# Kernel optimization log

Measured on AMD Instinct MI355X. Metric: run time of the kernel, lower is better.

Reference implementation:

```python
import jax, jax.numpy as jnp
import numpy as np

N_NODES = 8192
N_EDGES = 262144
IN_DIM = 256
HID = 256
OUT_DIM = 64
PATH_DIM = 64
N_HEADS = 4


def setup_inputs() -> dict:
    key = jax.random.key(0)
    ks = jax.random.split(key, 16)
    s = 0.05
    x = jax.random.normal(ks[0], (N_NODES, IN_DIM), dtype=jnp.float32)
    edge_index = jax.random.randint(ks[1], (2, N_EDGES), 0, N_NODES, dtype=jnp.int32)
    return {
        "x": x,
        "edge_index": edge_index,
        # pathway encoder Linear(IN_DIM, PATH_DIM)
        "pe_w": jax.random.normal(ks[2], (IN_DIM, PATH_DIM), jnp.float32) * s,
        "pe_b": jax.random.normal(ks[3], (PATH_DIM,), jnp.float32) * s,
        # MultiheadAttention packed in-proj [3E, E] and out-proj [E, E]
        "in_proj_w": jax.random.normal(ks[4], (3 * PATH_DIM, PATH_DIM), jnp.float32) * s,
        "in_proj_b": jax.random.normal(ks[5], (3 * PATH_DIM,), jnp.float32) * s,
        "out_proj_w": jax.random.normal(ks[6], (PATH_DIM, PATH_DIM), jnp.float32) * s,
        "out_proj_b": jax.random.normal(ks[7], (PATH_DIM,), jnp.float32) * s,
        # GCN layer weights (in_dim, out_dim) + bias
        "w1": jax.random.normal(ks[8], (IN_DIM + PATH_DIM, HID), jnp.float32) * s,
        "b1": jax.random.normal(ks[9], (HID,), jnp.float32) * s,
        "w2": jax.random.normal(ks[10], (HID, HID), jnp.float32) * s,
        "b2": jax.random.normal(ks[11], (HID,), jnp.float32) * s,
        "w3": jax.random.normal(ks[12], (HID, OUT_DIM), jnp.float32) * s,
        "b3": jax.random.normal(ks[13], (OUT_DIM,), jnp.float32) * s,
    }


def mha_self(x, in_proj_w, in_proj_b, out_proj_w, out_proj_b):
    # unbatched nn.MultiheadAttention: x [N, E], Q=K=V=x
    N, E = x.shape
    dh = E // N_HEADS
    qkv = x @ in_proj_w.T + in_proj_b  # [N, 3E]
    q, k, v = jnp.split(qkv, 3, axis=-1)
    # [H, N, dh]
    q = q.reshape(N, N_HEADS, dh).transpose(1, 0, 2)
    k = k.reshape(N, N_HEADS, dh).transpose(1, 0, 2)
    v = v.reshape(N, N_HEADS, dh).transpose(1, 0, 2)
    scores = jnp.einsum('hnd,hmd->hnm', q, k) / jnp.sqrt(jnp.float32(dh))
    attn = jax.nn.softmax(scores, axis=-1)
    out = jnp.einsum('hnm,hmd->hnd', attn, v)  # [H, N, dh]
    out = out.transpose(1, 0, 2).reshape(N, E)
    return out @ out_proj_w.T + out_proj_b


def gcn_conv(h, edge_index, w, b, num_nodes):
    # PyG GCNConv: add self loops, symmetric normalization, linear, scatter-add, bias
    src = jnp.concatenate([edge_index[0], jnp.arange(num_nodes, dtype=edge_index.dtype)])
    dst = jnp.concatenate([edge_index[1], jnp.arange(num_nodes, dtype=edge_index.dtype)])
    deg = jax.ops.segment_sum(jnp.ones_like(dst, dtype=h.dtype), dst, num_segments=num_nodes)
    dinv = jnp.where(deg > 0, jax.lax.rsqrt(jnp.maximum(deg, 1e-12)), 0.0)
    hw = h @ w  # [N, out]
    norm = (dinv[src] * dinv[dst])[:, None]
    msg = hw[src] * norm
    out = jax.ops.segment_sum(msg, dst, num_segments=num_nodes)
    return out + b


def reference(x, edge_index, pe_w, pe_b, in_proj_w, in_proj_b, out_proj_w, out_proj_b,
              w1, b1, w2, b2, w3, b3):
    N = x.shape[0]
    pf = x @ pe_w + pe_b  # pathway encoder
    pa = mha_self(pf, in_proj_w, in_proj_b, out_proj_w, out_proj_b)
    h = jnp.concatenate([x, pa], axis=-1)  # [N, IN_DIM + PATH_DIM]
    h = jax.nn.relu(gcn_conv(h, edge_index, w1, b1, N))  # dropout is identity (eval)
    h = jax.nn.relu(gcn_conv(h, edge_index, w2, b2, N))
    h = gcn_conv(h, edge_index, w3, b3, N)
    return h
```

## Files before the change

kernel.cpp:

```cpp
#include <hip/hip_runtime.h>
#include <hip/hip_bf16.h>

#define N_NODES 8192
#define N_EDGES 262144
#define IN_DIM 256
#define HID 256
#define OUT_DIM 64
#define PATH_DIM 64
#define NHEADS 4
#define DH 16
#define KSPLIT 8
#define SPLIT_KEYS (N_NODES / KSPLIT)
#define NITER (SPLIT_KEYS / 64)

typedef __attribute__((ext_vector_type(8))) short bf16x8;
typedef __attribute__((ext_vector_type(4))) short bf16x4;
typedef __attribute__((ext_vector_type(4))) float f32x4;

__device__ __forceinline__ ushort f2bf(float f) {
  union { float f; unsigned int u; } c;
  c.f = f;
  unsigned int u = c.u;
  u += 0x7fffu + ((u >> 16) & 1u);
  return (ushort)(u >> 16);
}

__device__ __forceinline__ float bf2f(ushort u) {
  union { float f; unsigned int u; } c;
  c.u = ((unsigned int)u) << 16;
  return c.f;
}

__device__ __forceinline__ float fast_exp2(float x) {
  float r;
  asm("v_exp_f32 %0, %1" : "=v"(r) : "v"(x));
  return r;
}

__device__ __forceinline__ unsigned pack_bf16(float a, float b) {
  union { __hip_bfloat162 h; unsigned u; } c;
  c.h = __float22bfloat162_rn(make_float2(a, b));
  return c.u;
}

#if __has_builtin(__builtin_amdgcn_mfma_f32_16x16x16bf16_1k)
__device__ __forceinline__ f32x4 mfma16(bf16x4 a, bf16x4 b, f32x4 c) {
  return __builtin_amdgcn_mfma_f32_16x16x16bf16_1k(a, b, c, 0, 0, 0);
}
#else
__device__ __forceinline__ f32x4 mfma16(bf16x4 a, bf16x4 b, f32x4 c) {
  f32x4 d;
  asm volatile("v_mfma_f32_16x16x16_bf16 %0, %1, %2, %3\n\ts_nop 7\n\ts_nop 3"
               : "=v"(d) : "v"(a), "v"(b), "v"(c));
  return d;
}
#endif


__global__ __launch_bounds__(256) void init_graph(int* deg, int* cursor) {
  int i = blockIdx.x * 256 + threadIdx.x;
  if (i < N_NODES) { deg[i] = 1; cursor[i] = 0; }
}

__global__ __launch_bounds__(256) void count_deg(const int* __restrict__ dst,
                                                 int* __restrict__ deg) {
  int e = blockIdx.x * 256 + threadIdx.x;
  if (e < N_EDGES) atomicAdd(&deg[dst[e]], 1);
}

__global__ __launch_bounds__(256) void scan_rows(const int* __restrict__ deg,
                                                 int* __restrict__ row_off,
                                                 float* __restrict__ dinv) {
  __shared__ int part[256];
  int t = threadIdx.x;
  int base = t * 32;
  int local[32];
  int s = 0;
  #pragma unroll
  for (int i = 0; i < 32; ++i) {
    int c = deg[base + i] - 1;
    local[i] = s;
    s += c;
  }
  part[t] = s;
  __syncthreads();
  for (int d = 1; d < 256; d <<= 1) {
    int v = (t >= d) ? part[t - d] : 0;
    __syncthreads();
    part[t] += v;
    __syncthreads();
  }
  int prev = (t == 0) ? 0 : part[t - 1];
  #pragma unroll
  for (int i = 0; i < 32; ++i) {
    row_off[base + i] = prev + local[i];
    dinv[base + i] = rsqrtf((float)deg[base + i]);
  }
}

__global__ __launch_bounds__(256) void fill_csr(const int* __restrict__ src,
                                                const int* __restrict__ dst,
                                                const int* __restrict__ row_off,
                                                int* __restrict__ cursor,
                                                int* __restrict__ csr) {
  int e = blockIdx.x * 256 + threadIdx.x;
  if (e < N_EDGES) {
    int d = dst[e];
    int p = atomicAdd(&cursor[d], 1);
    csr[row_off[d] + p] = src[e];
  }
}


__global__ __launch_bounds__(256) void transpose_w(const float* __restrict__ W,
                                                   float* __restrict__ Wt,
                                                   int R, int C) {
  int i = blockIdx.x * 256 + threadIdx.x;
  if (i < R * C) {
    int r = i / C, c = i % C;
    Wt[c * R + r] = W[i];
  }
}

__global__ __launch_bounds__(256) void convert_wsplit(const float* __restrict__ W,
                                                      ushort* __restrict__ Bthi,
                                                      ushort* __restrict__ Btlo,
                                                      int K, int N) {
  int i = blockIdx.x * 256 + threadIdx.x;
  if (i < K * N) {
    int k = i / N, n = i % N;
    float v = W[i];
    ushort hi = f2bf(v);
    ushort lo = f2bf(v - bf2f(hi));
    Bthi[(size_t)n * K + k] = hi;
    Btlo[(size_t)n * K + k] = lo;
  }
}

__global__ __launch_bounds__(256) void convert_xpa(const float* __restrict__ x,
                                                   const float* __restrict__ pa,
                                                   ushort* __restrict__ Axpa) {
  int i = blockIdx.x * 256 + threadIdx.x;
  int n = i / 80;
  int c = (i % 80) * 4;
  float4 v;
  if (c < 256)
    v = *reinterpret_cast<const float4*>(x + (size_t)n * 256 + c);
  else
    v = *reinterpret_cast<const float4*>(pa + (size_t)n * 64 + (c - 256));
  *reinterpret_cast<ushort4*>(Axpa + (size_t)n * 320 + c) =
      make_ushort4(f2bf(v.x), f2bf(v.y), f2bf(v.z), f2bf(v.w));
}

__global__ __launch_bounds__(256) void convert_qkv(const float* __restrict__ qkv,
                                                   ushort* __restrict__ Qbf,
                                                   ushort* __restrict__ Kbf,
                                                   ushort* __restrict__ Vtb) {
  const int tg = blockIdx.x * 256 + threadIdx.x;
  const int h = tg >> 13;
  const int n = tg & 8191;
  const float SC = 0.36067376022224085f;
  const float* base = qkv + (size_t)n * 192 + h * 16;
  ushort* qd = Qbf + ((size_t)h * 8192 + n) * 32;
  ushort* kd = Kbf + ((size_t)h * 8192 + n) * 32;
  ushort4 zz = make_ushort4(0, 0, 0, 0);
  #pragma unroll
  for (int i = 0; i < 16; i += 4) {
    float4 q4 = *reinterpret_cast<const float4*>(base + i);
    float4 k4 = *reinterpret_cast<const float4*>(base + 64 + i);
    float4 v4 = *reinterpret_cast<const float4*>(base + 128 + i);
    *reinterpret_cast<ushort4*>(qd + i) =
        make_ushort4(f2bf(q4.x * SC), f2bf(q4.y * SC), f2bf(q4.z * SC), f2bf(q4.w * SC));
    *reinterpret_cast<ushort4*>(kd + i) =
        make_ushort4(f2bf(k4.x), f2bf(k4.y), f2bf(k4.z), f2bf(k4.w));
    *reinterpret_cast<ushort4*>(qd + 16 + i) = zz;
    *reinterpret_cast<ushort4*>(kd + 16 + i) = zz;
    Vtb[((size_t)h * 16 + i + 0) * 8192 + n] = f2bf(v4.x);
    Vtb[((size_t)h * 16 + i + 1) * 8192 + n] = f2bf(v4.y);
    Vtb[((size_t)h * 16 + i + 2) * 8192 + n] = f2bf(v4.z);
    Vtb[((size_t)h * 16 + i + 3) * 8192 + n] = f2bf(v4.w);
  }
}


template <bool RELU, bool BIAS>
__global__ __launch_bounds__(256) void gemm_tile(const float* __restrict__ A1, int K1,
                                                 const float* __restrict__ A2, int K2,
                                                 const float* __restrict__ B,
                                                 const float* __restrict__ bias,
                                                 float* __restrict__ C, int N) {
  __shared__ __align__(16) float As[16][64];
  __shared__ __align__(16) float Bs[16][68];
  const int K = K1 + K2;
  const int bm = blockIdx.y * 64;
  const int bn = blockIdx.x * 64;
  const int t = threadIdx.x;
  const int tx = t & 15, ty = t >> 4;
  const int am = t >> 2;
  const int ak = (t & 3) << 2;
  const int bk = t >> 4;
  const int bn4 = (t & 15) << 2;
  float acc[4][4] = {};
  for (int k0 = 0; k0 < K; k0 += 16) {
    int kk = k0 + ak;
    int row = bm + am;
    float4 av;
    if (kk < K1)
      av = *reinterpret_cast<const float4*>(A1 + (size_t)row * K1 + kk);
    else
      av = *reinterpret_cast<const float4*>(A2 + (size_t)row * K2 + (kk - K1));
    As[ak + 0][am] = av.x;
    As[ak + 1][am] = av.y;
    As[ak + 2][am] = av.z;
    As[ak + 3][am] = av.w;
    float4 bv = *reinterpret_cast<const float4*>(B + (size_t)(k0 + bk) * N + bn + bn4);
    *reinterpret_cast<float4*>(&Bs[bk][bn4]) = bv;
    __syncthreads();
    #pragma unroll
    for (int k = 0; k < 16; ++k) {
      float4 a = *reinterpret_cast<const float4*>(&As[k][ty << 2]);
      float4 b = *reinterpret_cast<const float4*>(&Bs[k][tx << 2]);
      acc[0][0] += a.x * b.x; acc[0][1] += a.x * b.y; acc[0][2] += a.x * b.z; acc[0][3] += a.x * b.w;
      acc[1][0] += a.y * b.x; acc[1][1] += a.y * b.y; acc[1][2] += a.y * b.z; acc[1][3] += a.y * b.w;
      acc[2][0] += a.z * b.x; acc[2][1] += a.z * b.y; acc[2][2] += a.z * b.z; acc[2][3] += a.z * b.w;
      acc[3][0] += a.w * b.x; acc[3][1] += a.w * b.y; acc[3][2] += a.w * b.z; acc[3][3] += a.w * b.w;
    }
    __syncthreads();
  }
  #pragma unroll
  for (int i = 0; i < 4; ++i) {
    int row = bm + (ty << 2) + i;
    float4 o = make_float4(acc[i][0], acc[i][1], acc[i][2], acc[i][3]);
    if (BIAS) {
      float4 bv = *reinterpret_cast<const float4*>(bias + bn + (tx << 2));
      o.x += bv.x; o.y += bv.y; o.z += bv.z; o.w += bv.w;
    }
    if (RELU) {
      o.x = fmaxf(o.x, 0.f); o.y = fmaxf(o.y, 0.f);
      o.z = fmaxf(o.z, 0.f); o.w = fmaxf(o.w, 0.f);
    }
    *reinterpret_cast<float4*>(C + (size_t)row * N + bn + (tx << 2)) = o;
  }
}


template <int K, int NT>
__global__ __launch_bounds__(256) void gemm_mfma(const ushort* __restrict__ A,
                                                 const ushort* __restrict__ Bthi,
                                                 const ushort* __restrict__ Btlo,
                                                 ushort* __restrict__ C) {
  const int t = threadIdx.x;
  const int wv = t >> 6;
  const int l = t & 63;
  const int lg = l >> 4;
  const int lc = l & 15;
  const int bm = blockIdx.y * 64;
  const int n = blockIdx.x * 64 + wv * 16 + lc;

  const ushort* ap = A + (size_t)(bm + lc) * K + lg * 8;
  const ushort* bh = Bthi + (size_t)n * K + lg * 8;
  const ushort* bl = Btlo + (size_t)n * K + lg * 8;

  f32x4 acc[4] = {{0.f,0.f,0.f,0.f},{0.f,0.f,0.f,0.f},{0.f,0.f,0.f,0.f},{0.f,0.f,0.f,0.f}};
  #pragma unroll 2
  for (int k0 = 0; k0 < K; k0 += 32) {
    bf16x8 vh = *reinterpret_cast<const bf16x8*>(bh + k0);
    bf16x8 vl = *reinterpret_cast<const bf16x8*>(bl + k0);
    #pragma unroll
    for (int mt = 0; mt < 4; ++mt) {
      bf16x8 af = *reinterpret_cast<const bf16x8*>(ap + (size_t)mt * 16 * K + k0);
      acc[mt] = __builtin_amdgcn_mfma_f32_16x16x32_bf16(af, vh, acc[mt], 0, 0, 0);
      acc[mt] = __builtin_amdgcn_mfma_f32_16x16x32_bf16(af, vl, acc[mt], 0, 0, 0);
    }
  }
  #pragma unroll
  for (int mt = 0; mt < 4; ++mt) {
    #pragma unroll
    for (int r = 0; r < 4; ++r)
      C[(size_t)(bm + mt * 16 + lg * 4 + r) * NT + n] = f2bf(acc[mt][r]);
  }
}


__global__ __launch_bounds__(256) void attn_mfma5(const ushort* __restrict__ Qbf,
                                                  const ushort* __restrict__ Kbf,
                                                  const ushort* __restrict__ Vtb,
                                                  float* __restrict__ Opart,
                                                  float* __restrict__ Wpart) {
  const int h  = blockIdx.y;
  const int qb = blockIdx.x;
  const int kz = blockIdx.z;
  const int t  = threadIdx.x;
  const int wv = t >> 6;
  const int l  = t & 63;
  const int lg = l >> 4;
  const int lc = l & 15;

  __shared__ float red_o[3][64][17];
  __shared__ float red_w[3][64];

  bf16x8 qf[4];
  {
    const ushort* qbase = Qbf + ((size_t)h * 8192 + qb * 64) * 32;
    #pragma unroll
    for (int qt = 0; qt < 4; ++qt)
      qf[qt] = *reinterpret_cast<const bf16x8*>(qbase + (qt * 16 + lc) * 32 + lg * 8);
  }

  const ushort* kptr =
      Kbf + ((size_t)h * 8192 + kz * SPLIT_KEYS + wv * 16 + lc) * 32 + lg * 8;
  const ushort* vptr =
      Vtb + ((size_t)h * 16 + lc) * 8192 + kz * SPLIT_KEYS + wv * 16 + lg * 4;

  f32x4 oacc[4] = {{0.f, 0.f, 0.f, 0.f}, {0.f, 0.f, 0.f, 0.f},
                   {0.f, 0.f, 0.f, 0.f}, {0.f, 0.f, 0.f, 0.f}};
  float wsum[4] = {0.f, 0.f, 0.f, 0.f};

  bf16x8 kf = *reinterpret_cast<const bf16x8*>(kptr);
  bf16x4 vf = *reinterpret_cast<const bf16x4*>(vptr);

  for (int c = 0; c < NITER; ++c) {
    bf16x8 kf_n;
    bf16x4 vf_n;
    if (c + 1 < NITER) {
      kf_n = *reinterpret_cast<const bf16x8*>(kptr + (size_t)(c + 1) * 64 * 32);
      vf_n = *reinterpret_cast<const bf16x4*>(vptr + (size_t)(c + 1) * 64);
    }

    f32x4 s[4];
    #pragma unroll
    for (int qt = 0; qt < 4; ++qt) {
      f32x4 z = {0.f, 0.f, 0.f, 0.f};
      s[qt] = __builtin_amdgcn_mfma_f32_16x16x32_bf16(kf, qf[qt], z, 0, 0, 0);
    }

    #pragma unroll
    for (int qt = 0; qt < 4; ++qt) {
      float e0 = fast_exp2(s[qt][0]);
      float e1 = fast_exp2(s[qt][1]);
      float e2 = fast_exp2(s[qt][2]);
      float e3 = fast_exp2(s[qt][3]);
      wsum[qt] += (e0 + e1) + (e2 + e3);
      union { uint2 u; bf16x4 v; } pu;
      pu.u.x = pack_bf16(e0, e1);
      pu.u.y = pack_bf16(e2, e3);
      oacc[qt] = mfma16(pu.v, vf, oacc[qt]);
    }

    kf = kf_n;
    vf = vf_n;
  }

  #pragma unroll
  for (int qt = 0; qt < 4; ++qt) {
    float v = wsum[qt];
    v += __shfl_xor(v, 16);
    v += __shfl_xor(v, 32);
    wsum[qt] = v;
  }

  if (wv > 0) {
    #pragma unroll
    for (int qt = 0; qt < 4; ++qt) {
      #pragma unroll
      for (int r = 0; r < 4; ++r)
        red_o[wv - 1][qt * 16 + lg * 4 + r][lc] = oacc[qt][r];
      if (lg == 0) red_w[wv - 1][qt * 16 + lc] = wsum[qt];
    }
  }
  __syncthreads();

  if (wv == 0) {
    const size_t obase = ((size_t)(kz * NHEADS + h) * N_NODES + qb * 64);
    #pragma unroll
    for (int qt = 0; qt < 4; ++qt) {
      #pragma unroll
      for (int r = 0; r < 4; ++r) {
        const int q = qt * 16 + lg * 4 + r;
        float o = oacc[qt][r] + red_o[0][q][lc] + red_o[1][q][lc] + red_o[2][q][lc];
        Opart[(obase + q) * 16 + lc] = o;
      }
      if (lg == 0) {
        const int q = qt * 16 + lc;
        Wpart[obase + q] = wsum[qt] + red_w[0][q] + red_w[1][q] + red_w[2][q];
      }
    }
  }
}

__global__ __launch_bounds__(256) void attn_combine(const float* __restrict__ Opart,
                                                    const float* __restrict__ Wpart,
                                                    float* __restrict__ attn_out) {
  int i = blockIdx.x * 256 + threadIdx.x;
  int dq = i & 3;
  int hn = i >> 2;
  int h = hn >> 13;
  int n = hn & 8191;
  float4 acc = make_float4(0.f, 0.f, 0.f, 0.f);
  float ws = 0.f;
  #pragma unroll
  for (int s = 0; s < KSPLIT; ++s) {
    const size_t row = ((size_t)(s * NHEADS + h) * N_NODES + n);
    float4 v = *reinterpret_cast<const float4*>(Opart + row * 16 + dq * 4);
    acc.x += v.x; acc.y += v.y; acc.z += v.z; acc.w += v.w;
    ws += Wpart[row];
  }
  float inv = 1.f / ws;
  float4 o = make_float4(acc.x * inv, acc.y * inv, acc.z * inv, acc.w * inv);
  *reinterpret_cast<float4*>(attn_out + (size_t)n * 64 + h * 16 + dq * 4) = o;
}


template <bool RELU, bool OUTBF>
__global__ __launch_bounds__(256) void aggregate_bf(const ushort* __restrict__ hwb,
                                                    const int* __restrict__ csr,
                                                    const int* __restrict__ row_off,
                                                    const int* __restrict__ deg,
                                                    const float* __restrict__ dinv,
                                                    const float* __restrict__ bias,
                                                    ushort* __restrict__ outb,
                                                    float* __restrict__ outf) {
  __shared__ __align__(16) float part[2][256];
  const int t = threadIdx.x;
  const int rw = t >> 7;
  const int wh = (t >> 6) & 1;
  const int l = t & 63;
  const int r = blockIdx.x * 2 + rw;
  const float dr = dinv[r];
  const int off = row_off[r];
  const int cnt = deg[r] - 1;
  const int c = l << 2;

  float a0, a1, a2, a3;
  if (wh == 0) {
    ushort4 u = *reinterpret_cast<const ushort4*>(hwb + (size_t)r * 256 + c);
    a0 = dr * bf2f(u.x); a1 = dr * bf2f(u.y); a2 = dr * bf2f(u.z); a3 = dr * bf2f(u.w);
  } else {
    a0 = a1 = a2 = a3 = 0.f;
  }
  for (int e = wh; e < cnt; e += 2) {
    int s = csr[off + e];
    float wsc = dinv[s];
    ushort4 u = *reinterpret_cast<const ushort4*>(hwb + (size_t)s * 256 + c);
    a0 += wsc * bf2f(u.x); a1 += wsc * bf2f(u.y);
    a2 += wsc * bf2f(u.z); a3 += wsc * bf2f(u.w);
  }
  if (wh == 1)
    *reinterpret_cast<float4*>(&part[rw][c]) = make_float4(a0, a1, a2, a3);
  __syncthreads();
  if (wh == 0) {
    float4 p = *reinterpret_cast<const float4*>(&part[rw][c]);
    float4 bv = *reinterpret_cast<const float4*>(bias + c);
    float o0 = dr * (a0 + p.x) + bv.x;
    float o1 = dr * (a1 + p.y) + bv.y;
    float o2 = dr * (a2 + p.z) + bv.z;
    float o3 = dr * (a3 + p.w) + bv.w;
    if (RELU) {
      o0 = fmaxf(o0, 0.f); o1 = fmaxf(o1, 0.f);
      o2 = fmaxf(o2, 0.f); o3 = fmaxf(o3, 0.f);
    }
    if (OUTBF) {
      *reinterpret_cast<ushort4*>(outb + (size_t)r * 256 + c) =
          make_ushort4(f2bf(o0), f2bf(o1), f2bf(o2), f2bf(o3));
    } else {
      *reinterpret_cast<float4*>(outf + (size_t)r * 256 + c) =
          make_float4(o0, o1, o2, o3);
    }
  }
}

__global__ __launch_bounds__(256) void aggregate64_bf(const ushort* __restrict__ hwb,
                                                      const int* __restrict__ csr,
                                                      const int* __restrict__ row_off,
                                                      const int* __restrict__ deg,
                                                      const float* __restrict__ dinv,
                                                      const float* __restrict__ bias,
                                                      float* __restrict__ out) {
  const int w = threadIdx.x >> 6, l = threadIdx.x & 63;
  const int r = blockIdx.x * 4 + w;
  const float dr = dinv[r];
  const int off = row_off[r];
  const int cnt = deg[r] - 1;
  float a = dr * bf2f(hwb[(size_t)r * 64 + l]);
  for (int e = 0; e < cnt; ++e) {
    int s = csr[off + e];
    a += dinv[s] * bf2f(hwb[(size_t)s * 64 + l]);
  }
  out[(size_t)r * 64 + l] = dr * a + bias[l];
}


extern "C" void kernel_launch(void* const* d_in, const int* in_sizes, int n_in,
                              void* d_out, int out_size, void* d_ws, size_t ws_size,
                              hipStream_t stream) {
  const float* x          = (const float*)d_in[0];
  const int*   ei         = (const int*)d_in[1];
  const float* pe_w       = (const float*)d_in[2];
  const float* pe_b       = (const float*)d_in[3];
  const float* in_proj_w  = (const float*)d_in[4];
  const float* in_proj_b  = (const float*)d_in[5];
  const float* out_proj_w = (const float*)d_in[6];
  const float* out_proj_b = (const float*)d_in[7];
  const float* w1         = (const float*)d_in[8];
  const float* b1         = (const float*)d_in[9];
  const float* w2         = (const float*)d_in[10];
  const float* b2         = (const float*)d_in[11];
  const float* w3         = (const float*)d_in[12];
  const float* b3         = (const float*)d_in[13];

  const int* esrc = ei;
  const int* edst = ei + N_EDGES;

  char* ws = (char*)d_ws;
  size_t o = 0;
  auto take = [&](size_t n) {
    char* p = ws + o;
    o += (n + 255) & ~(size_t)255;
    return p;
  };
  float* pf       = (float*)take((size_t)N_NODES * PATH_DIM * 4);
  float* qkv      = (float*)take((size_t)N_NODES * 3 * PATH_DIM * 4);
  float* attn_out = (float*)take((size_t)N_NODES * PATH_DIM * 4);
  float* pa       = (float*)take((size_t)N_NODES * PATH_DIM * 4);
  char*  region1  = take(18874368);
  ushort* Qbf     = (ushort*)take((size_t)NHEADS * N_NODES * 32 * 2);
  ushort* Kbf     = (ushort*)take((size_t)NHEADS * N_NODES * 32 * 2);
  ushort* Vtb     = (ushort*)take((size_t)NHEADS * DH * N_NODES * 2);
  ushort* Bt1hi   = (ushort*)take((size_t)HID * 320 * 2);
  ushort* Bt1lo   = (ushort*)take((size_t)HID * 320 * 2);
  ushort* Bt2hi   = (ushort*)take((size_t)HID * HID * 2);
  ushort* Bt2lo   = (ushort*)take((size_t)HID * HID * 2);
  ushort* Bt3hi   = (ushort*)take((size_t)OUT_DIM * HID * 2);
  ushort* Bt3lo   = (ushort*)take((size_t)OUT_DIM * HID * 2);
  float* Wt_in    = (float*)take((size_t)3 * PATH_DIM * PATH_DIM * 4);
  float* Wt_out   = (float*)take((size_t)PATH_DIM * PATH_DIM * 4);
  float* dinv     = (float*)take((size_t)N_NODES * 4);
  int*   deg      = (int*)take((size_t)N_NODES * 4);
  int*   cursor   = (int*)take((size_t)N_NODES * 4);
  int*   row_off  = (int*)take((size_t)N_NODES * 4);
  int*   csr      = (int*)take((size_t)N_EDGES * 4);

  float* Opart = (float*)region1;
  float* Wpart = (float*)(region1 + 16777216);
  ushort* Axpa  = (ushort*)region1;
  ushort* hwbf  = Axpa + (size_t)N_NODES * 320;
  ushort* h1bf  = hwbf + (size_t)N_NODES * 256;
  ushort* h2bf  = h1bf + (size_t)N_NODES * 256;
  ushort* hw64  = h2bf + (size_t)N_NODES * 256;

  init_graph<<<N_NODES / 256, 256, 0, stream>>>(deg, cursor);
  count_deg<<<N_EDGES / 256, 256, 0, stream>>>(edst, deg);
  scan_rows<<<1, 256, 0, stream>>>(deg, row_off, dinv);
  fill_csr<<<N_EDGES / 256, 256, 0, stream>>>(esrc, edst, row_off, cursor, csr);

  transpose_w<<<(192 * 64 + 255) / 256, 256, 0, stream>>>(in_proj_w, Wt_in, 192, 64);
  transpose_w<<<(64 * 64 + 255) / 256, 256, 0, stream>>>(out_proj_w, Wt_out, 64, 64);
  convert_wsplit<<<(320 * 256 + 255) / 256, 256, 0, stream>>>(w1, Bt1hi, Bt1lo, 320, HID);
  convert_wsplit<<<(256 * 256 + 255) / 256, 256, 0, stream>>>(w2, Bt2hi, Bt2lo, HID, HID);
  convert_wsplit<<<(256 * 64 + 255) / 256, 256, 0, stream>>>(w3, Bt3hi, Bt3lo, HID, OUT_DIM);

  gemm_tile<false, true><<<dim3(1, 128), 256, 0, stream>>>(x, IN_DIM, nullptr, 0, pe_w, pe_b, pf, PATH_DIM);
  gemm_tile<false, true><<<dim3(3, 128), 256, 0, stream>>>(pf, PATH_DIM, nullptr, 0, Wt_in, in_proj_b, qkv, 3 * PATH_DIM);
  convert_qkv<<<(N_NODES * NHEADS) / 256, 256, 0, stream>>>(qkv, Qbf, Kbf, Vtb);
  attn_mfma5<<<dim3(128, 4, KSPLIT), 256, 0, stream>>>(Qbf, Kbf, Vtb, Opart, Wpart);
  attn_combine<<<(NHEADS * N_NODES * 4) / 256, 256, 0, stream>>>(Opart, Wpart, attn_out);
  gemm_tile<false, true><<<dim3(1, 128), 256, 0, stream>>>(attn_out, PATH_DIM, nullptr, 0, Wt_out, out_proj_b, pa, PATH_DIM);

  convert_xpa<<<(N_NODES * 80) / 256, 256, 0, stream>>>(x, pa, Axpa);
  gemm_mfma<320, 256><<<dim3(4, 128), 256, 0, stream>>>(Axpa, Bt1hi, Bt1lo, hwbf);
  aggregate_bf<true, true><<<N_NODES / 2, 256, 0, stream>>>(hwbf, csr, row_off, deg, dinv, b1, h1bf, nullptr);
  gemm_mfma<256, 256><<<dim3(4, 128), 256, 0, stream>>>(h1bf, Bt2hi, Bt2lo, hwbf);
  aggregate_bf<true, true><<<N_NODES / 2, 256, 0, stream>>>(hwbf, csr, row_off, deg, dinv, b2, h2bf, nullptr);
  gemm_mfma<256, 64><<<dim3(1, 128), 256, 0, stream>>>(h2bf, Bt3hi, Bt3lo, hw64);
  aggregate64_bf<<<N_NODES / 4, 256, 0, stream>>>(hw64, csr, row_off, deg, dinv, b3, (float*)d_out);
}
```

Before: 275.1 us.

## Fold pathway encoder into QKV projection and fuse prep and combine kernels

Pre-multiplies pe_w by in_proj_w, scaling the Q columns, so one GEMM from x produces Q/K/V directly in bf16 attention layouts. This drops the pf GEMM and the convert_qkv pass. The attention split-K combine is fused into the out-projection GEMM, which writes bf16 straight into the Axpa columns. Weight transposes and conversions plus the x-to-bf16 conversion are merged into a single prep launch. This cuts launches and intermediate fp32 round trips, but the QKV GEMM now has K=256 instead of 64 and the algebraic reassociation slightly changes rounding.

```diff
diff --git a/kernel.cpp b/kernel.cpp
--- a/kernel.cpp
+++ b/kernel.cpp
@@ -112,108 +112,96 @@
 }
 
 
-__global__ __launch_bounds__(256) void transpose_w(const float* __restrict__ W,
-                                                   float* __restrict__ Wt,
-                                                   int R, int C) {
-  int i = blockIdx.x * 256 + threadIdx.x;
-  if (i < R * C) {
-    int r = i / C, c = i % C;
-    Wt[c * R + r] = W[i];
-  }
-}
-
-__global__ __launch_bounds__(256) void convert_wsplit(const float* __restrict__ W,
-                                                      ushort* __restrict__ Bthi,
-                                                      ushort* __restrict__ Btlo,
-                                                      int K, int N) {
-  int i = blockIdx.x * 256 + threadIdx.x;
-  if (i < K * N) {
-    int k = i / N, n = i % N;
-    float v = W[i];
+__global__ __launch_bounds__(256) void prep(const float* __restrict__ x,
+                                            const float* __restrict__ pe_w,
+                                            const float* __restrict__ pe_b,
+                                            const float* __restrict__ in_proj_w,
+                                            const float* __restrict__ in_proj_b,
+                                            const float* __restrict__ out_proj_w,
+                                            const float* __restrict__ w1,
+                                            const float* __restrict__ w2,
+                                            const float* __restrict__ w3,
+                                            ushort* __restrict__ Axpa,
+                                            float* __restrict__ Wpp,
+                                            float* __restrict__ bpp,
+                                            float* __restrict__ WtO,
+                                            ushort* __restrict__ Bt1hi, ushort* __restrict__ Bt1lo,
+                                            ushort* __restrict__ Bt2hi, ushort* __restrict__ Bt2lo,
+                                            ushort* __restrict__ Bt3hi, ushort* __restrict__ Bt3lo) {
+  const float SC = 0.36067376022224085f;
+  const int b = blockIdx.x;
+  const int t = threadIdx.x;
+  if (b < 2048) {
+    int e = b * 256 + t;
+    int n = e >> 6, qi = (e & 63) << 2;
+    float4 v = *reinterpret_cast<const float4*>(x + (size_t)n * 256 + qi);
+    *reinterpret_cast<ushort4*>(Axpa + (size_t)n * 320 + qi) =
+        make_ushort4(f2bf(v.x), f2bf(v.y), f2bf(v.z), f2bf(v.w));
+  } else if (b < 2240) {
+    int e = (b - 2048) * 256 + t;
+    int k = e / 192, c = e % 192;
+    float s = 0.f;
+    for (int j = 0; j < 64; ++j) s += pe_w[k * 64 + j] * in_proj_w[c * 64 + j];
+    if (c < 64) s *= SC;
+    Wpp[k * 192 + c] = s;
+  } else if (b == 2240) {
+    if (t < 192) {
+      float s = 0.f;
+      for (int j = 0; j < 64; ++j) s += pe_b[j] * in_proj_w[t * 64 + j];
+      s += in_proj_b[t];
+      if (t < 64) s *= SC;
+      bpp[t] = s;
+    }
+  } else if (b < 2257) {
+    int e = (b - 2241) * 256 + t;
+    int r = e >> 6, c = e & 63;
+    WtO[c * 64 + r] = out_proj_w[e];
+  } else if (b < 2577) {
+    int e = (b - 2257) * 256 + t;
+    int k = e >> 8, n = e & 255;
+    float v = w1[e];
     ushort hi = f2bf(v);
-    ushort lo = f2bf(v - bf2f(hi));
-    Bthi[(size_t)n * K + k] = hi;
-    Btlo[(size_t)n * K + k] = lo;
-  }
-}
-
-__global__ __launch_bounds__(256) void convert_xpa(const float* __restrict__ x,
-                                                   const float* __restrict__ pa,
-                                                   ushort* __restrict__ Axpa) {
-  int i = blockIdx.x * 256 + threadIdx.x;
-  int n = i / 80;
-  int c = (i % 80) * 4;
-  float4 v;
-  if (c < 256)
-    v = *reinterpret_cast<const float4*>(x + (size_t)n * 256 + c);
-  else
-    v = *reinterpret_cast<const float4*>(pa + (size_t)n * 64 + (c - 256));
-  *reinterpret_cast<ushort4*>(Axpa + (size_t)n * 320 + c) =
-      make_ushort4(f2bf(v.x), f2bf(v.y), f2bf(v.z), f2bf(v.w));
-}
-
-__global__ __launch_bounds__(256) void convert_qkv(const float* __restrict__ qkv,
-                                                   ushort* __restrict__ Qbf,
-                                                   ushort* __restrict__ Kbf,
-                                                   ushort* __restrict__ Vtb) {
-  const int tg = blockIdx.x * 256 + threadIdx.x;
-  const int h = tg >> 13;
-  const int n = tg & 8191;
-  const float SC = 0.36067376022224085f;
-  const float* base = qkv + (size_t)n * 192 + h * 16;
-  ushort* qd = Qbf + ((size_t)h * 8192 + n) * 32;
-  ushort* kd = Kbf + ((size_t)h * 8192 + n) * 32;
-  ushort4 zz = make_ushort4(0, 0, 0, 0);
-  #pragma unroll
-  for (int i = 0; i < 16; i += 4) {
-    float4 q4 = *reinterpret_cast<const float4*>(base + i);
-    float4 k4 = *reinterpret_cast<const float4*>(base + 64 + i);
-    float4 v4 = *reinterpret_cast<const float4*>(base + 128 + i);
-    *reinterpret_cast<ushort4*>(qd + i) =
-        make_ushort4(f2bf(q4.x * SC), f2bf(q4.y * SC), f2bf(q4.z * SC), f2bf(q4.w * SC));
-    *reinterpret_cast<ushort4*>(kd + i) =
-        make_ushort4(f2bf(k4.x), f2bf(k4.y), f2bf(k4.z), f2bf(k4.w));
-    *reinterpret_cast<ushort4*>(qd + 16 + i) = zz;
-    *reinterpret_cast<ushort4*>(kd + 16 + i) = zz;
-    Vtb[((size_t)h * 16 + i + 0) * 8192 + n] = f2bf(v4.x);
-    Vtb[((size_t)h * 16 + i + 1) * 8192 + n] = f2bf(v4.y);
-    Vtb[((size_t)h * 16 + i + 2) * 8192 + n] = f2bf(v4.z);
-    Vtb[((size_t)h * 16 + i + 3) * 8192 + n] = f2bf(v4.w);
-  }
-}
-
-
-template <bool RELU, bool BIAS>
-__global__ __launch_bounds__(256) void gemm_tile(const float* __restrict__ A1, int K1,
-                                                 const float* __restrict__ A2, int K2,
-                                                 const float* __restrict__ B,
-                                                 const float* __restrict__ bias,
-                                                 float* __restrict__ C, int N) {
+    Bt1hi[(size_t)n * 320 + k] = hi;
+    Bt1lo[(size_t)n * 320 + k] = f2bf(v - bf2f(hi));
+  } else if (b < 2833) {
+    int e = (b - 2577) * 256 + t;
+    int k = e >> 8, n = e & 255;
+    float v = w2[e];
+    ushort hi = f2bf(v);
+    Bt2hi[(size_t)n * 256 + k] = hi;
+    Bt2lo[(size_t)n * 256 + k] = f2bf(v - bf2f(hi));
+  } else {
+    int e = (b - 2833) * 256 + t;
+    int k = e >> 6, n = e & 63;
+    float v = w3[e];
+    ushort hi = f2bf(v);
+    Bt3hi[(size_t)n * 256 + k] = hi;
+    Bt3lo[(size_t)n * 256 + k] = f2bf(v - bf2f(hi));
+  }
+}
+
+
+__global__ __launch_bounds__(256) void gemm_qkv(const float* __restrict__ x,
+                                                const float* __restrict__ Wpp,
+                                                const float* __restrict__ bpp,
+                                                ushort* __restrict__ Qbf,
+                                                ushort* __restrict__ Kbf,
+                                                ushort* __restrict__ Vtb) {
   __shared__ __align__(16) float As[16][64];
   __shared__ __align__(16) float Bs[16][68];
-  const int K = K1 + K2;
   const int bm = blockIdx.y * 64;
-  const int bn = blockIdx.x * 64;
+  const int bx = blockIdx.x;
+  const int bn = bx * 64;
   const int t = threadIdx.x;
   const int tx = t & 15, ty = t >> 4;
-  const int am = t >> 2;
-  const int ak = (t & 3) << 2;
-  const int bk = t >> 4;
-  const int bn4 = (t & 15) << 2;
+  const int am = t >> 2, ak = (t & 3) << 2;
+  const int bk = t >> 4, bn4 = (t & 15) << 2;
   float acc[4][4] = {};
-  for (int k0 = 0; k0 < K; k0 += 16) {
-    int kk = k0 + ak;
-    int row = bm + am;
-    float4 av;
-    if (kk < K1)
-      av = *reinterpret_cast<const float4*>(A1 + (size_t)row * K1 + kk);
-    else
-      av = *reinterpret_cast<const float4*>(A2 + (size_t)row * K2 + (kk - K1));
-    As[ak + 0][am] = av.x;
-    As[ak + 1][am] = av.y;
-    As[ak + 2][am] = av.z;
-    As[ak + 3][am] = av.w;
-    float4 bv = *reinterpret_cast<const float4*>(B + (size_t)(k0 + bk) * N + bn + bn4);
+  for (int k0 = 0; k0 < 256; k0 += 16) {
+    float4 av = *reinterpret_cast<const float4*>(x + (size_t)(bm + am) * 256 + k0 + ak);
+    As[ak + 0][am] = av.x; As[ak + 1][am] = av.y;
+    As[ak + 2][am] = av.z; As[ak + 3][am] = av.w;
+    float4 bv = *reinterpret_cast<const float4*>(Wpp + (size_t)(k0 + bk) * 192 + bn + bn4);
     *reinterpret_cast<float4*>(&Bs[bk][bn4]) = bv;
     __syncthreads();
     #pragma unroll
@@ -227,57 +215,28 @@
     }
     __syncthreads();
   }
+  const int cl = tx << 2;
+  const int h = cl >> 4, d = cl & 15;
+  float4 bb = *reinterpret_cast<const float4*>(bpp + bn + cl);
+  const ushort4 zz = make_ushort4(0, 0, 0, 0);
   #pragma unroll
   for (int i = 0; i < 4; ++i) {
     int row = bm + (ty << 2) + i;
-    float4 o = make_float4(acc[i][0], acc[i][1], acc[i][2], acc[i][3]);
-    if (BIAS) {
-      float4 bv = *reinterpret_cast<const float4*>(bias + bn + (tx << 2));
-      o.x += bv.x; o.y += bv.y; o.z += bv.z; o.w += bv.w;
-    }
-    if (RELU) {
-      o.x = fmaxf(o.x, 0.f); o.y = fmaxf(o.y, 0.f);
-      o.z = fmaxf(o.z, 0.f); o.w = fmaxf(o.w, 0.f);
-    }
-    *reinterpret_cast<float4*>(C + (size_t)row * N + bn + (tx << 2)) = o;
-  }
-}
-
-
-template <int K, int NT>
-__global__ __launch_bounds__(256) void gemm_mfma(const ushort* __restrict__ A,
-                                                 const ushort* __restrict__ Bthi,
-                                                 const ushort* __restrict__ Btlo,
-                                                 ushort* __restrict__ C) {
-  const int t = threadIdx.x;
-  const int wv = t >> 6;
-  const int l = t & 63;
-  const int lg = l >> 4;
-  const int lc = l & 15;
-  const int bm = blockIdx.y * 64;
-  const int n = blockIdx.x * 64 + wv * 16 + lc;
-
-  const ushort* ap = A + (size_t)(bm + lc) * K + lg * 8;
-  const ushort* bh = Bthi + (size_t)n * K + lg * 8;
-  const ushort* bl = Btlo + (size_t)n * K + lg * 8;
-
-  f32x4 acc[4] = {{0.f,0.f,0.f,0.f},{0.f,0.f,0.f,0.f},{0.f,0.f,0.f,0.f},{0.f,0.f,0.f,0.f}};
-  #pragma unroll 2
-  for (int k0 = 0; k0 < K; k0 += 32) {
-    bf16x8 vh = *reinterpret_cast<const bf16x8*>(bh + k0);
-    bf16x8 vl = *reinterpret_cast<const bf16x8*>(bl + k0);
-    #pragma unroll
-    for (int mt = 0; mt < 4; ++mt) {
-      bf16x8 af = *reinterpret_cast<const bf16x8*>(ap + (size_t)mt * 16 * K + k0);
-      acc[mt] = __builtin_amdgcn_mfma_f32_16x16x32_bf16(af, vh, acc[mt], 0, 0, 0);
-      acc[mt] = __builtin_amdgcn_mfma_f32_16x16x32_bf16(af, vl, acc[mt], 0, 0, 0);
-    }
-  }
-  #pragma unroll
-  for (int mt = 0; mt < 4; ++mt) {
-    #pragma unroll
-    for (int r = 0; r < 4; ++r)
-      C[(size_t)(bm + mt * 16 + lg * 4 + r) * NT + n] = f2bf(acc[mt][r]);
+    float o0 = acc[i][0] + bb.x, o1 = acc[i][1] + bb.y;
+    float o2 = acc[i][2] + bb.z, o3 = acc[i][3] + bb.w;
+    ushort4 u = make_ushort4(f2bf(o0), f2bf(o1), f2bf(o2), f2bf(o3));
+    if (bx == 0) {
+      *reinterpret_cast<ushort4*>(Qbf + ((size_t)h * 8192 + row) * 32 + d) = u;
+      *reinterpret_cast<ushort4*>(Qbf + ((size_t)h * 8192 + row) * 32 + d + 16) = zz;
+    } else if (bx == 1) {
+      *reinterpret_cast<ushort4*>(Kbf + ((size_t)h * 8192 + row) * 32 + d) = u;
+      *reinterpret_cast<ushort4*>(Kbf + ((size_t)h * 8192 + row) * 32 + d + 16) = zz;
+    } else {
+      Vtb[((size_t)h * 16 + d + 0) * 8192 + row] = u.x;
+      Vtb[((size_t)h * 16 + d + 1) * 8192 + row] = u.y;
+      Vtb[((size_t)h * 16 + d + 2) * 8192 + row] = u.z;
+      Vtb[((size_t)h * 16 + d + 3) * 8192 + row] = u.w;
+    }
   }
 }
 
@@ -388,38 +347,107 @@
   }
 }
 
-__global__ __launch_bounds__(256) void attn_combine(const float* __restrict__ Opart,
-                                                    const float* __restrict__ Wpart,
-                                                    float* __restrict__ attn_out) {
-  int i = blockIdx.x * 256 + threadIdx.x;
-  int dq = i & 3;
-  int hn = i >> 2;
-  int h = hn >> 13;
-  int n = hn & 8191;
-  float4 acc = make_float4(0.f, 0.f, 0.f, 0.f);
-  float ws = 0.f;
+
+__global__ __launch_bounds__(256) void gemm_pa(const float* __restrict__ Opart,
+                                               const float* __restrict__ Wpart,
+                                               const float* __restrict__ WtO,
+                                               const float* __restrict__ ob,
+                                               ushort* __restrict__ Axpa) {
+  __shared__ __align__(16) float As[16][64];
+  __shared__ __align__(16) float Bs[16][68];
+  const int bm = blockIdx.y * 64;
+  const int t = threadIdx.x;
+  const int tx = t & 15, ty = t >> 4;
+  const int am = t >> 2, ak = (t & 3) << 2;
+  const int bk = t >> 4, bn4 = (t & 15) << 2;
+  float acc[4][4] = {};
+  for (int k0 = 0; k0 < 64; k0 += 16) {
+    const int kk = k0 + ak;
+    const int row = bm + am;
+    const int h = kk >> 4, d = kk & 15;
+    float ax = 0.f, ay = 0.f, az = 0.f, aw = 0.f, ws = 0.f;
+    #pragma unroll
+    for (int s = 0; s < KSPLIT; ++s) {
+      const size_t rb = (size_t)(s * NHEADS + h) * N_NODES + row;
+      float4 v = *reinterpret_cast<const float4*>(Opart + rb * 16 + d);
+      ax += v.x; ay += v.y; az += v.z; aw += v.w;
+      ws += Wpart[rb];
+    }
+    float inv = 1.f / ws;
+    As[ak + 0][am] = ax * inv; As[ak + 1][am] = ay * inv;
+    As[ak + 2][am] = az * inv; As[ak + 3][am] = aw * inv;
+    float4 bv = *reinterpret_cast<const float4*>(WtO + (size_t)(k0 + bk) * 64 + bn4);
+    *reinterpret_cast<float4*>(&Bs[bk][bn4]) = bv;
+    __syncthreads();
+    #pragma unroll
+    for (int k = 0; k < 16; ++k) {
+      float4 a = *reinterpret_cast<const float4*>(&As[k][ty << 2]);
+      float4 b = *reinterpret_cast<const float4*>(&Bs[k][tx << 2]);
+      acc[0][0] += a.x * b.x; acc[0][1] += a.x * b.y; acc[0][2] += a.x * b.z; acc[0][3] += a.x * b.w;
+      acc[1][0] += a.y * b.x; acc[1][1] += a.y * b.y; acc[1][2] += a.y * b.z; acc[1][3] += a.y * b.w;
+      acc[2][0] += a.z * b.x; acc[2][1] += a.z * b.y; acc[2][2] += a.z * b.z; acc[2][3] += a.z * b.w;
+      acc[3][0] += a.w * b.x; acc[3][1] += a.w * b.y; acc[3][2] += a.w * b.z; acc[3][3] += a.w * b.w;
+    }
+    __syncthreads();
+  }
+  float4 bb = *reinterpret_cast<const float4*>(ob + (tx << 2));
   #pragma unroll
-  for (int s = 0; s < KSPLIT; ++s) {
-    const size_t row = ((size_t)(s * NHEADS + h) * N_NODES + n);
-    float4 v = *reinterpret_cast<const float4*>(Opart + row * 16 + dq * 4);
-    acc.x += v.x; acc.y += v.y; acc.z += v.z; acc.w += v.w;
-    ws += Wpart[row];
-  }
-  float inv = 1.f / ws;
-  float4 o = make_float4(acc.x * inv, acc.y * inv, acc.z * inv, acc.w * inv);
-  *reinterpret_cast<float4*>(attn_out + (size_t)n * 64 + h * 16 + dq * 4) = o;
-}
-
-
-template <bool RELU, bool OUTBF>
+  for (int i = 0; i < 4; ++i) {
+    int row = bm + (ty << 2) + i;
+    float o0 = acc[i][0] + bb.x, o1 = acc[i][1] + bb.y;
+    float o2 = acc[i][2] + bb.z, o3 = acc[i][3] + bb.w;
+    *reinterpret_cast<ushort4*>(Axpa + (size_t)row * 320 + 256 + (tx << 2)) =
+        make_ushort4(f2bf(o0), f2bf(o1), f2bf(o2), f2bf(o3));
+  }
+}
+
+
+template <int K, int NT>
+__global__ __launch_bounds__(256) void gemm_mfma(const ushort* __restrict__ A,
+                                                 const ushort* __restrict__ Bthi,
+                                                 const ushort* __restrict__ Btlo,
+                                                 ushort* __restrict__ C) {
+  const int t = threadIdx.x;
+  const int wv = t >> 6;
+  const int l = t & 63;
+  const int lg = l >> 4;
+  const int lc = l & 15;
+  const int bm = blockIdx.y * 64;
+  const int n = blockIdx.x * 64 + wv * 16 + lc;
+
+  const ushort* ap = A + (size_t)(bm + lc) * K + lg * 8;
+  const ushort* bh = Bthi + (size_t)n * K + lg * 8;
+  const ushort* bl = Btlo + (size_t)n * K + lg * 8;
+
+  f32x4 acc[4] = {{0.f,0.f,0.f,0.f},{0.f,0.f,0.f,0.f},{0.f,0.f,0.f,0.f},{0.f,0.f,0.f,0.f}};
+  #pragma unroll 2
+  for (int k0 = 0; k0 < K; k0 += 32) {
+    bf16x8 vh = *reinterpret_cast<const bf16x8*>(bh + k0);
+    bf16x8 vl = *reinterpret_cast<const bf16x8*>(bl + k0);
+    #pragma unroll
+    for (int mt = 0; mt < 4; ++mt) {
+      bf16x8 af = *reinterpret_cast<const bf16x8*>(ap + (size_t)mt * 16 * K + k0);
+      acc[mt] = __builtin_amdgcn_mfma_f32_16x16x32_bf16(af, vh, acc[mt], 0, 0, 0);
+      acc[mt] = __builtin_amdgcn_mfma_f32_16x16x32_bf16(af, vl, acc[mt], 0, 0, 0);
+    }
+  }
+  #pragma unroll
+  for (int mt = 0; mt < 4; ++mt) {
+    #pragma unroll
+    for (int r = 0; r < 4; ++r)
+      C[(size_t)(bm + mt * 16 + lg * 4 + r) * NT + n] = f2bf(acc[mt][r]);
+  }
+}
+
+
+template <bool RELU>
 __global__ __launch_bounds__(256) void aggregate_bf(const ushort* __restrict__ hwb,
                                                     const int* __restrict__ csr,
                                                     const int* __restrict__ row_off,
                                                     const int* __restrict__ deg,
                                                     const float* __restrict__ dinv,
                                                     const float* __restrict__ bias,
-                                                    ushort* __restrict__ outb,
-                                                    float* __restrict__ outf) {
+                                                    ushort* __restrict__ outb) {
   __shared__ __align__(16) float part[2][256];
   const int t = threadIdx.x;
   const int rw = t >> 7;
@@ -459,13 +487,8 @@
       o0 = fmaxf(o0, 0.f); o1 = fmaxf(o1, 0.f);
       o2 = fmaxf(o2, 0.f); o3 = fmaxf(o3, 0.f);
     }
-    if (OUTBF) {
-      *reinterpret_cast<ushort4*>(outb + (size_t)r * 256 + c) =
-          make_ushort4(f2bf(o0), f2bf(o1), f2bf(o2), f2bf(o3));
-    } else {
-      *reinterpret_cast<float4*>(outf + (size_t)r * 256 + c) =
-          make_float4(o0, o1, o2, o3);
-    }
+    *reinterpret_cast<ushort4*>(outb + (size_t)r * 256 + c) =
+        make_ushort4(f2bf(o0), f2bf(o1), f2bf(o2), f2bf(o3));
   }
 }
 
@@ -518,59 +541,50 @@
     o += (n + 255) & ~(size_t)255;
     return p;
   };
-  float* pf       = (float*)take((size_t)N_NODES * PATH_DIM * 4);
-  float* qkv      = (float*)take((size_t)N_NODES * 3 * PATH_DIM * 4);
-  float* attn_out = (float*)take((size_t)N_NODES * PATH_DIM * 4);
-  float* pa       = (float*)take((size_t)N_NODES * PATH_DIM * 4);
-  char*  region1  = take(18874368);
+  char*   region1 = take(18874368);
+  ushort* Axpa    = (ushort*)take((size_t)N_NODES * 320 * 2);
   ushort* Qbf     = (ushort*)take((size_t)NHEADS * N_NODES * 32 * 2);
   ushort* Kbf     = (ushort*)take((size_t)NHEADS * N_NODES * 32 * 2);
   ushort* Vtb     = (ushort*)take((size_t)NHEADS * DH * N_NODES * 2);
+  float*  Wpp     = (float*)take((size_t)256 * 192 * 4);
+  float*  bpp     = (float*)take((size_t)192 * 4);
+  float*  WtO     = (float*)take((size_t)64 * 64 * 4);
   ushort* Bt1hi   = (ushort*)take((size_t)HID * 320 * 2);
   ushort* Bt1lo   = (ushort*)take((size_t)HID * 320 * 2);
   ushort* Bt2hi   = (ushort*)take((size_t)HID * HID * 2);
   ushort* Bt2lo   = (ushort*)take((size_t)HID * HID * 2);
   ushort* Bt3hi   = (ushort*)take((size_t)OUT_DIM * HID * 2);
   ushort* Bt3lo   = (ushort*)take((size_t)OUT_DIM * HID * 2);
-  float* Wt_in    = (float*)take((size_t)3 * PATH_DIM * PATH_DIM * 4);
-  float* Wt_out   = (float*)take((size_t)PATH_DIM * PATH_DIM * 4);
-  float* dinv     = (float*)take((size_t)N_NODES * 4);
-  int*   deg      = (int*)take((size_t)N_NODES * 4);
-  int*   cursor   = (int*)take((size_t)N_NODES * 4);
-  int*   row_off  = (int*)take((size_t)N_NODES * 4);
-  int*   csr      = (int*)take((size_t)N_EDGES * 4);
+  float*  dinv    = (float*)take((size_t)N_NODES * 4);
+  int*    deg     = (int*)take((size_t)N_NODES * 4);
+  int*    cursor  = (int*)take((size_t)N_NODES * 4);
+  int*    row_off = (int*)take((size_t)N_NODES * 4);
+  int*    csr     = (int*)take((size_t)N_EDGES * 4);
 
   float* Opart = (float*)region1;
   float* Wpart = (float*)(region1 + 16777216);
-  ushort* Axpa  = (ushort*)region1;
-  ushort* hwbf  = Axpa + (size_t)N_NODES * 320;
-  ushort* h1bf  = hwbf + (size_t)N_NODES * 256;
-  ushort* h2bf  = h1bf + (size_t)N_NODES * 256;
-  ushort* hw64  = h2bf + (size_t)N_NODES * 256;
+  ushort* hwbf = (ushort*)region1;
+  ushort* h1bf = hwbf + (size_t)N_NODES * 256;
+  ushort* h2bf = h1bf + (size_t)N_NODES * 256;
+  ushort* hw64 = h2bf + (size_t)N_NODES * 256;
 
   init_graph<<<N_NODES / 256, 256, 0, stream>>>(deg, cursor);
   count_deg<<<N_EDGES / 256, 256, 0, stream>>>(edst, deg);
   scan_rows<<<1, 256, 0, stream>>>(deg, row_off, dinv);
   fill_csr<<<N_EDGES / 256, 256, 0, stream>>>(esrc, edst, row_off, cursor, csr);
 
-  transpose_w<<<(192 * 64 + 255) / 256, 256, 0, stream>>>(in_proj_w, Wt_in, 192, 64);
-  transpose_w<<<(64 * 64 + 255) / 256, 256, 0, stream>>>(out_proj_w, Wt_out, 64, 64);
-  convert_wsplit<<<(320 * 256 + 255) / 256, 256, 0, stream>>>(w1, Bt1hi, Bt1lo, 320, HID);
-  convert_wsplit<<<(256 * 256 + 255) / 256, 256, 0, stream>>>(w2, Bt2hi, Bt2lo, HID, HID);
-  convert_wsplit<<<(256 * 64 + 255) / 256, 256, 0, stream>>>(w3, Bt3hi, Bt3lo, HID, OUT_DIM);
-
-  gemm_tile<false, true><<<dim3(1, 128), 256, 0, stream>>>(x, IN_DIM, nullptr, 0, pe_w, pe_b, pf, PATH_DIM);
-  gemm_tile<false, true><<<dim3(3, 128), 256, 0, stream>>>(pf, PATH_DIM, nullptr, 0, Wt_in, in_proj_b, qkv, 3 * PATH_DIM);
-  convert_qkv<<<(N_NODES * NHEADS) / 256, 256, 0, stream>>>(qkv, Qbf, Kbf, Vtb);
+  prep<<<2897, 256, 0, stream>>>(x, pe_w, pe_b, in_proj_w, in_proj_b, out_proj_w,
+                                 w1, w2, w3, Axpa, Wpp, bpp, WtO,
+                                 Bt1hi, Bt1lo, Bt2hi, Bt2lo, Bt3hi, Bt3lo);
+
+  gemm_qkv<<<dim3(3, 128), 256, 0, stream>>>(x, Wpp, bpp, Qbf, Kbf, Vtb);
   attn_mfma5<<<dim3(128, 4, KSPLIT), 256, 0, stream>>>(Qbf, Kbf, Vtb, Opart, Wpart);
-  attn_combine<<<(NHEADS * N_NODES * 4) / 256, 256, 0, stream>>>(Opart, Wpart, attn_out);
-  gemm_tile<false, true><<<dim3(1, 128), 256, 0, stream>>>(attn_out, PATH_DIM, nullptr, 0, Wt_out, out_proj_b, pa, PATH_DIM);
-
-  convert_xpa<<<(N_NODES * 80) / 256, 256, 0, stream>>>(x, pa, Axpa);
+  gemm_pa<<<dim3(1, 128), 256, 0, stream>>>(Opart, Wpart, WtO, out_proj_b, Axpa);
+
   gemm_mfma<320, 256><<<dim3(4, 128), 256, 0, stream>>>(Axpa, Bt1hi, Bt1lo, hwbf);
-  aggregate_bf<true, true><<<N_NODES / 2, 256, 0, stream>>>(hwbf, csr, row_off, deg, dinv, b1, h1bf, nullptr);
+  aggregate_bf<true><<<N_NODES / 2, 256, 0, stream>>>(hwbf, csr, row_off, deg, dinv, b1, h1bf);
   gemm_mfma<256, 256><<<dim3(4, 128), 256, 0, stream>>>(h1bf, Bt2hi, Bt2lo, hwbf);
-  aggregate_bf<true, true><<<N_NODES / 2, 256, 0, stream>>>(hwbf, csr, row_off, deg, dinv, b2, h2bf, nullptr);
+  aggregate_bf<true><<<N_NODES / 2, 256, 0, stream>>>(hwbf, csr, row_off, deg, dinv, b2, h2bf);
   gemm_mfma<256, 64><<<dim3(1, 128), 256, 0, stream>>>(h2bf, Bt3hi, Bt3lo, hw64);
   aggregate64_bf<<<N_NODES / 4, 256, 0, stream>>>(hw64, csr, row_off, deg, dinv, b3, (float*)d_out);
 }
```

Result: no change. 279.2 us (+1.5%).
